# Performance work log

Hardware: AMD Instinct MI355X
Metric: run time of the kernel (lower is better)

## Reference

```python
import jax, jax.numpy as jnp
import numpy as np

B, H, W, C = 16, 56, 56, 512
HEADS, WIN = 16, 7
HID = 2048
EPS = 1e-5


def _rel_pos_index(win):
    coords = np.stack(np.meshgrid(np.arange(win), np.arange(win), indexing='ij'))  # 2,w,w
    cf = coords.reshape(2, -1)  # 2, w*w
    rel = (cf[:, :, None] - cf[:, None, :]).transpose(1, 2, 0).astype(np.int64)  # N,N,2
    rel[..., 0] += win - 1
    rel[..., 1] += win - 1
    rel[..., 0] *= 2 * win - 1
    return jnp.asarray(rel.sum(-1))  # N,N


def setup_inputs() -> dict:
    key = jax.random.key(0)
    ks = jax.random.split(key, 12)
    s = 0.02
    return {
        'x': jax.random.normal(ks[0], (B, H * W, C), jnp.float32),
        'norm1_w': jnp.ones((C,), jnp.float32),
        'norm1_b': jnp.zeros((C,), jnp.float32),
        'qkv_w': jax.random.normal(ks[1], (3 * C, C), jnp.float32) * s,
        'qkv_b': jnp.zeros((3 * C,), jnp.float32),
        'proj_w': jax.random.normal(ks[2], (C, C), jnp.float32) * s,
        'proj_b': jnp.zeros((C,), jnp.float32),
        'rel_bias_table': jax.random.normal(ks[3], ((2 * WIN - 1) ** 2, HEADS), jnp.float32) * s,
        'norm2_w': jnp.ones((C,), jnp.float32),
        'norm2_b': jnp.zeros((C,), jnp.float32),
        'fc1_w': jax.random.normal(ks[4], (HID, C), jnp.float32) * s,
        'fc1_b': jnp.zeros((HID,), jnp.float32),
        'fc2_w': jax.random.normal(ks[5], (C, HID), jnp.float32) * s,
        'fc2_b': jnp.zeros((C,), jnp.float32),
        'rel_pos_index': _rel_pos_index(WIN),
    }


def _ln(x, w, b):
    m = jnp.mean(x, -1, keepdims=True)
    v = jnp.mean((x - m) ** 2, -1, keepdims=True)
    return (x - m) * jax.lax.rsqrt(v + EPS) * w + b


def reference(x, norm1_w, norm1_b, qkv_w, qkv_b, proj_w, proj_b, rel_bias_table,
              norm2_w, norm2_b, fc1_w, fc1_b, fc2_w, fc2_b, rel_pos_index):
    N = WIN * WIN
    hd = C // HEADS
    shortcut = x
    h = _ln(x, norm1_w, norm1_b).reshape(B, H, W, C)
    # window partition -> (nW*B, N, C)
    h = h.reshape(B, H // WIN, WIN, W // WIN, WIN, C).transpose(0, 1, 3, 2, 4, 5)
    xw = h.reshape(-1, N, C)
    Bw = xw.shape[0]
    qkv = (xw @ qkv_w.T + qkv_b).reshape(Bw, N, 3, HEADS, hd).transpose(2, 0, 3, 1, 4)
    q, k, v = qkv[0], qkv[1], qkv[2]  # (Bw, heads, N, hd)
    q = q * (hd ** -0.5)
    attn = jnp.einsum('bhnd,bhmd->bhnm', q, k)
    bias = rel_bias_table[rel_pos_index.reshape(-1)].reshape(N, N, HEADS).transpose(2, 0, 1)
    attn = jax.nn.softmax(attn + bias[None], axis=-1)
    out = jnp.einsum('bhnm,bhmd->bhnd', attn, v).transpose(0, 2, 1, 3).reshape(Bw, N, C)
    out = out @ proj_w.T + proj_b
    # window reverse -> (B, H*W, C)
    out = out.reshape(B, H // WIN, W // WIN, WIN, WIN, C).transpose(0, 1, 3, 2, 4, 5)
    out = out.reshape(B, H * W, C)
    x = shortcut + out
    h2 = _ln(x, norm2_w, norm2_b)
    h2 = jax.nn.gelu(h2 @ fc1_w.T + fc1_b, approximate=False) @ fc2_w.T + fc2_b
    return x + h2
```

## Files before the change

### kernel.cpp

```cpp
#include <hip/hip_runtime.h>
#include <stdint.h>

#define B_    16
#define C_    512
#define HEADS 16
#define NTOK  49
#define ROWS  (16*56*56)

typedef __attribute__((ext_vector_type(8))) __bf16 bf16x8;
typedef __attribute__((ext_vector_type(4))) float  f32x4;
typedef __attribute__((ext_vector_type(8))) unsigned short u16x8;
typedef __attribute__((ext_vector_type(4))) unsigned short u16x4;

#define AS1 __attribute__((address_space(1)))
#define AS3 __attribute__((address_space(3)))

__device__ __forceinline__ unsigned short f2bf(float f) {
  union { float f; uint32_t u; } x; x.f = f;
  uint32_t r = x.u + 0x7FFFu + ((x.u >> 16) & 1u);
  return (unsigned short)(r >> 16);
}
__device__ __forceinline__ float bf2f(unsigned short u) {
  union { uint32_t u; float f; } x; x.u = ((uint32_t)u) << 16;
  return x.f;
}

__device__ __forceinline__ int winmap(int grow) {
  const int b = grow / 3136;
  const int pos = grow - b * 3136;
  const int y = pos / 56, x = pos - y * 56;
  const int win = (y / 7) * 8 + (x / 7);
  const int r = (y % 7) * 7 + (x % 7);
  return b * 3136 + win * 49 + r;
}

template<int EPI, int GATHER>
__global__ __launch_bounds__(256, 4)
void gemm_bt(const unsigned short* __restrict__ A,
             const unsigned short* __restrict__ Bt,
             const float* __restrict__ bias,
             const float* __restrict__ res,
             void* __restrict__ outp,
             int N, int K, int ldb, int nbn)
{
  __shared__ __align__(16) unsigned short As[2][128*32];
  __shared__ __align__(16) unsigned short Bs[2][128*32];

  const int nwg = gridDim.x;
  const int q8 = nwg >> 3, r8 = nwg & 7;
  const int xcd = blockIdx.x & 7, ixc = blockIdx.x >> 3;
  const int l = (xcd < r8 ? xcd * (q8 + 1) : r8 * (q8 + 1) + (xcd - r8) * q8) + ixc;
  const int bm = l / nbn, bn = l % nbn;

  const int tid  = threadIdx.x;
  const int wave = tid >> 6;
  const int lane = tid & 63;
  const int wr = wave >> 1, wc = wave & 1;

  const unsigned short* aSrc[2];
  const unsigned short* bSrc[2];
  #pragma unroll
  for (int i = 0; i < 2; ++i) {
    const int u = tid + i * 256;
    const int srow = u >> 2;
    const int sg   = (u & 3) ^ ((srow >> 1) & 3);
    int ga = bm * 128 + srow;
    if (GATHER) ga = winmap(ga);
    aSrc[i] = A  + (size_t)ga * K + sg * 8;
    bSrc[i] = Bt + (size_t)(bn * 128 + srow) * ldb + sg * 8;
  }

  f32x4 acc[4][4] = {};
  const int fr = lane & 15;
  const int kq = lane >> 4;
  const int xrd = kq ^ ((fr >> 1) & 3);

  auto STAGE = [&](int buf, int t) {
    const int k0 = t << 5;
    #pragma unroll
    for (int i = 0; i < 2; ++i)
      __builtin_amdgcn_global_load_lds(
        (const AS1 void*)(aSrc[i] + k0),
        (AS3 void*)(&As[buf][(i * 256 + wave * 64) * 8]), 16, 0, 0);
    #pragma unroll
    for (int i = 0; i < 2; ++i)
      __builtin_amdgcn_global_load_lds(
        (const AS1 void*)(bSrc[i] + k0),
        (AS3 void*)(&Bs[buf][(i * 256 + wave * 64) * 8]), 16, 0, 0);
  };

  const int nt = K >> 5;
  STAGE(0, 0);
  for (int t = 0; t < nt; ++t) {
    const int c = t & 1;
    if (t + 1 < nt) {
      STAGE(c ^ 1, t + 1);
      asm volatile("s_waitcnt vmcnt(4)" ::: "memory");
    } else {
      asm volatile("s_waitcnt vmcnt(0)" ::: "memory");
    }
    __builtin_amdgcn_s_barrier();
    asm volatile("" ::: "memory");

    bf16x8 a[4], b[4];
    #pragma unroll
    for (int m = 0; m < 4; ++m)
      a[m] = *(const bf16x8*)&As[c][(wr * 64 + m * 16 + fr) * 32 + xrd * 8];
    #pragma unroll
    for (int n = 0; n < 4; ++n)
      b[n] = *(const bf16x8*)&Bs[c][(wc * 64 + n * 16 + fr) * 32 + xrd * 8];

    __builtin_amdgcn_s_setprio(1);
    #pragma unroll
    for (int m = 0; m < 4; ++m)
      #pragma unroll
      for (int n = 0; n < 4; ++n)
        acc[m][n] = __builtin_amdgcn_mfma_f32_16x16x32_bf16(a[m], b[n], acc[m][n], 0, 0, 0);
    __builtin_amdgcn_s_setprio(0);

    asm volatile("s_waitcnt lgkmcnt(0)" ::: "memory");
    __builtin_amdgcn_s_barrier();
    asm volatile("" ::: "memory");
  }

  const int rq = lane >> 4;
  #pragma unroll
  for (int m = 0; m < 4; ++m) {
    #pragma unroll
    for (int n = 0; n < 4; ++n) {
      const int gcol = bn * 128 + wc * 64 + n * 16 + fr;
      const float bv = (EPI == 3) ? 0.f : bias[gcol];
      #pragma unroll
      for (int r = 0; r < 4; ++r) {
        const int grow = bm * 128 + wr * 64 + m * 16 + rq * 4 + r;
        const size_t off = (size_t)grow * N + gcol;
        float v = acc[m][n][r] + bv;
        if (EPI == 0) {
          ((unsigned short*)outp)[off] = f2bf(v);
        } else if (EPI == 1) {
          const float u2 = 1.5957691216f * v * (1.0f + 0.044715f * v * v);
          v = v / (1.0f + __expf(-u2));
          ((unsigned short*)outp)[off] = f2bf(v);
        } else {
          ((float*)outp)[off] = v + res[off];
        }
      }
    }
  }
}

__global__ __launch_bounds__(256)
void ln_bf16(const float* __restrict__ x, const float* __restrict__ w,
             const float* __restrict__ b, unsigned short* __restrict__ out)
{
  const int row  = blockIdx.x * 4 + (threadIdx.x >> 6);
  const int lane = threadIdx.x & 63;
  const float4* xr = (const float4*)(x + (size_t)row * C_);
  const float4 u = xr[lane * 2];
  const float4 v = xr[lane * 2 + 1];
  const float vals[8] = {u.x,u.y,u.z,u.w,v.x,v.y,v.z,v.w};
  float s = 0.f, s2 = 0.f;
  #pragma unroll
  for (int j = 0; j < 8; ++j) { s += vals[j]; s2 += vals[j]*vals[j]; }
  #pragma unroll
  for (int off = 1; off < 64; off <<= 1) {
    s  += __shfl_xor(s,  off);
    s2 += __shfl_xor(s2, off);
  }
  const float mean = s * (1.0f/512.0f);
  const float rstd = rsqrtf(s2 * (1.0f/512.0f) - mean*mean + 1e-5f);
  u16x8 o;
  #pragma unroll
  for (int j = 0; j < 8; ++j) {
    const int col = lane * 8 + j;
    o[j] = f2bf((vals[j] - mean) * rstd * w[col] + b[col]);
  }
  *(u16x8*)&out[(size_t)row * C_ + lane * 8] = o;
}

__global__ __launch_bounds__(256)
void attn_win3(const unsigned short* __restrict__ qkv,
               const unsigned short* __restrict__ biasBf,
               unsigned short* __restrict__ woutb, int i0)
{
  __shared__ float Ksh[4][NTOK*32];
  __shared__ float Vsh[4][NTOK*32];
  __shared__ unsigned short Bsh[4][NTOK*NTOK];
  const int bi = blockIdx.x;
  const int qtr = bi & 3, winl = bi >> 2;
  const int bbl = winl >> 6, wy = (winl >> 3) & 7, wx = winl & 7;
  const int wave = threadIdx.x >> 6, lane = threadIdx.x & 63;
  const int head = qtr * 4 + wave;

  for (int i = lane; i < NTOK*NTOK; i += 64)
    Bsh[wave][i] = biasBf[head * (NTOK*NTOK) + i];

  float q[32];
  if (lane < NTOK) {
    const int r = lane / 7, c = lane % 7;
    const size_t gl = (size_t)bbl * 3136 + (size_t)((wy*7 + r) * 56 + (wx*7 + c));
    const unsigned short* qp = qkv + gl * 1536 + head * 32;
    #pragma unroll
    for (int d = 0; d < 32; d += 4) {
      const u16x4 qv = *(const u16x4*)&qp[d];
      const u16x4 kv = *(const u16x4*)&qp[512 + d];
      const u16x4 vv = *(const u16x4*)&qp[1024 + d];
      #pragma unroll
      for (int e = 0; e < 4; ++e) {
        q[d+e] = bf2f(qv[e]);
        Ksh[wave][lane*32 + d + e] = bf2f(kv[e]);
        Vsh[wave][lane*32 + d + e] = bf2f(vv[e]);
      }
    }
  }
  if (lane < NTOK) {
    float lsum = 0.f;
    float o[32];
    #pragma unroll
    for (int d = 0; d < 32; ++d) o[d] = 0.f;
    for (int j = 0; j < NTOK; ++j) {
      float dot = 0.f;
      #pragma unroll
      for (int d = 0; d < 32; ++d) dot += q[d] * Ksh[wave][j*32 + d];
      const float val = dot * 0.17677669529663687f
                      + bf2f(Bsh[wave][lane*NTOK + j]);
      const float e = __expf(val);
      lsum += e;
      #pragma unroll
      for (int d = 0; d < 32; ++d) o[d] += e * Vsh[wave][j*32 + d];
    }
    const float inv = 1.0f / lsum;
    unsigned short* op = woutb
        + ((size_t)((bbl + i0) * 64 + wy * 8 + wx) * 49 + lane) * 512 + head * 32;
    #pragma unroll
    for (int d = 0; d < 32; d += 4) {
      u16x4 ov;
      #pragma unroll
      for (int e = 0; e < 4; ++e) ov[e] = f2bf(o[d+e] * inv);
      *(u16x4*)&op[d] = ov;
    }
  }
}

__global__ void build_bias(const float* __restrict__ table, const int* __restrict__ idx,
                           unsigned short* __restrict__ biasBf)
{
  const int i = blockIdx.x * 256 + threadIdx.x;
  if (i >= HEADS * NTOK * NTOK) return;
  const int h  = i / (NTOK*NTOK);
  const int ij = i - h * (NTOK*NTOK);
  biasBf[i] = f2bf(table[idx[ij] * HEADS + h]);
}

__global__ void conv_bf16(const float* __restrict__ in, unsigned short* __restrict__ out, int n4)
{
  const int i = blockIdx.x * 256 + threadIdx.x;
  if (i >= n4) return;
  const float4 v = ((const float4*)in)[i];
  u16x4 o; o[0]=f2bf(v.x); o[1]=f2bf(v.y); o[2]=f2bf(v.z); o[3]=f2bf(v.w);
  ((u16x4*)out)[i] = o;
}

extern "C" void kernel_launch(void* const* d_in, const int* in_sizes, int n_in,
                              void* d_out, int out_size, void* d_ws, size_t ws_size,
                              hipStream_t stream)
{
  const float* x     = (const float*)d_in[0];
  const float* n1w   = (const float*)d_in[1];
  const float* n1b   = (const float*)d_in[2];
  const float* qkvw  = (const float*)d_in[3];
  const float* qkvb  = (const float*)d_in[4];
  const float* projw = (const float*)d_in[5];
  const float* projb = (const float*)d_in[6];
  const float* rbt   = (const float*)d_in[7];
  const float* n2w   = (const float*)d_in[8];
  const float* n2b   = (const float*)d_in[9];
  const float* fc1w  = (const float*)d_in[10];
  const float* fc1b  = (const float*)d_in[11];
  const float* fc2w  = (const float*)d_in[12];
  const float* fc2b  = (const float*)d_in[13];
  const int*   rpi   = (const int*)d_in[14];
  float* out = (float*)d_out;

  char* p = (char*)d_ws;
  auto alloc = [&](size_t bytes) -> char* {
    char* q = p; p += (bytes + 255) & ~(size_t)255; return q;
  };
  unsigned short* wqB  = (unsigned short*)alloc((size_t)1536 * 512 * 2);
  unsigned short* wpB  = (unsigned short*)alloc((size_t)512  * 512 * 2);
  unsigned short* w1B  = (unsigned short*)alloc((size_t)2048 * 512 * 2);
  unsigned short* w2B  = (unsigned short*)alloc((size_t)512  * 2048 * 2);
  unsigned short* biasBf = (unsigned short*)alloc((size_t)HEADS * NTOK * NTOK * 2);
  unsigned short* bufX = (unsigned short*)alloc((size_t)ROWS * 512 * 2);
  const size_t used = (size_t)(p - (char*)d_ws);
  const size_t Rbytes = (ws_size > used) ? ws_size - used : 0;
  unsigned short* R = (unsigned short*)p;

  int ic = 0;
  for (int c = 16; c >= 2; c >>= 1)
    if ((size_t)c * 3136 * 1536 * 2 <= Rbytes) { ic = c; break; }
  int hc = 0;
  for (int c = 2048; c >= 128; c >>= 1)
    if ((size_t)ROWS * c * 2 <= Rbytes) { hc = c; break; }
  if (ic == 0 || hc == 0) return;

  conv_bf16<<<(1536*512/4 + 255)/256, 256, 0, stream>>>(qkvw, wqB, 1536*512/4);
  conv_bf16<<<(512*512/4  + 255)/256, 256, 0, stream>>>(projw, wpB, 512*512/4);
  conv_bf16<<<(2048*512/4 + 255)/256, 256, 0, stream>>>(fc1w, w1B, 2048*512/4);
  conv_bf16<<<(512*2048/4 + 255)/256, 256, 0, stream>>>(fc2w, w2B, 512*2048/4);
  build_bias<<<(HEADS*NTOK*NTOK + 255)/256, 256, 0, stream>>>(rbt, rpi, biasBf);

  ln_bf16<<<ROWS/4, 256, 0, stream>>>(x, n1w, n1b, bufX);

  for (int i0 = 0; i0 < B_; i0 += ic) {
    const int nbm = ic * 3136 / 128, nbn = 12;
    gemm_bt<0,0><<<nbm * nbn, 256, 0, stream>>>(
        bufX + (size_t)i0*3136*512, wqB, qkvb, nullptr, R, 1536, 512, 512, nbn);
    attn_win3<<<ic*64*4, 256, 0, stream>>>(R, biasBf, bufX, i0);
  }

  gemm_bt<2,1><<<(ROWS/128) * 4, 256, 0, stream>>>(
      bufX, wpB, projb, x, out, 512, 512, 512, 4);

  ln_bf16<<<ROWS/4, 256, 0, stream>>>(out, n2w, n2b, bufX);

  for (int h0 = 0; h0 < 2048; h0 += hc) {
    gemm_bt<1,0><<<(ROWS/128) * (hc/128), 256, 0, stream>>>(
        bufX, w1B + (size_t)h0*512, fc1b + h0, nullptr, R, hc, 512, 512, hc/128);
    if (h0 == 0)
      gemm_bt<2,0><<<(ROWS/128) * 4, 256, 0, stream>>>(
          R, w2B + h0, fc2b, out, out, 512, hc, 2048, 4);
    else
      gemm_bt<3,0><<<(ROWS/128) * 4, 256, 0, stream>>>(
          R, w2B + h0, nullptr, out, out, 512, hc, 2048, 4);
  }
}
```

Baseline: 717.9 us.

## Enlarge GEMM tiles to 256x256 with 8 waves and phased K=64 pipeline

The bf16 GEMM moves from 128x128 tiles with 4 waves and K-step 32 to 256x256 tiles with 8 waves (512 threads) and K-step 64. Each step is split into four phases that interleave LDS fragment reads, async global-to-LDS prefetch of the next stage, and MFMA blocks, with barriers between phases. The aim is more data reuse per loaded byte and better overlap of memory traffic with matrix math. In exchange it uses more LDS and registers (the acc array doubles), launches fewer workgroups, and adds more barriers. Host launch grids and chunk-size minimums are updated to match.

Result: slower. 759.1 us (+5.7%).

```diff
diff --git a/kernel.cpp b/kernel.cpp
--- a/kernel.cpp
+++ b/kernel.cpp
@@ -35,7 +35,7 @@
 }
 
 template<int EPI, int GATHER>
-__global__ __launch_bounds__(256, 4)
+__global__ __launch_bounds__(512, 2)
 void gemm_bt(const unsigned short* __restrict__ A,
              const unsigned short* __restrict__ Bt,
              const float* __restrict__ bias,
@@ -43,8 +43,8 @@
              void* __restrict__ outp,
              int N, int K, int ldb, int nbn)
 {
-  __shared__ __align__(16) unsigned short As[2][128*32];
-  __shared__ __align__(16) unsigned short Bs[2][128*32];
+  __shared__ __align__(16) unsigned short As[2][2 * 8192];
+  __shared__ __align__(16) unsigned short Bs[2][2 * 8192];
 
   const int nwg = gridDim.x;
   const int q8 = nwg >> 3, r8 = nwg & 7;
@@ -55,84 +55,102 @@
   const int tid  = threadIdx.x;
   const int wave = tid >> 6;
   const int lane = tid & 63;
-  const int wr = wave >> 1, wc = wave & 1;
-
-  const unsigned short* aSrc[2];
-  const unsigned short* bSrc[2];
+  const int wr = wave >> 2, wc = wave & 3;
+
+  const unsigned short* aP[2];
+  const unsigned short* bP[2];
   #pragma unroll
   for (int i = 0; i < 2; ++i) {
-    const int u = tid + i * 256;
-    const int srow = u >> 2;
-    const int sg   = (u & 3) ^ ((srow >> 1) & 3);
-    int ga = bm * 128 + srow;
+    const int u = i * 512 + tid;
+    const int row = u >> 2;
+    const int g = (u & 3) ^ ((row >> 1) & 3);
+    int ga = bm * 256 + row;
     if (GATHER) ga = winmap(ga);
-    aSrc[i] = A  + (size_t)ga * K + sg * 8;
-    bSrc[i] = Bt + (size_t)(bn * 128 + srow) * ldb + sg * 8;
-  }
-
-  f32x4 acc[4][4] = {};
+    aP[i] = A  + (size_t)ga * K + g * 8;
+    bP[i] = Bt + (size_t)(bn * 256 + row) * ldb + g * 8;
+  }
+
+  f32x4 acc[8][4] = {};
   const int fr = lane & 15;
   const int kq = lane >> 4;
   const int xrd = kq ^ ((fr >> 1) & 3);
 
-  auto STAGE = [&](int buf, int t) {
-    const int k0 = t << 5;
-    #pragma unroll
-    for (int i = 0; i < 2; ++i)
-      __builtin_amdgcn_global_load_lds(
-        (const AS1 void*)(aSrc[i] + k0),
-        (AS3 void*)(&As[buf][(i * 256 + wave * 64) * 8]), 16, 0, 0);
-    #pragma unroll
-    for (int i = 0; i < 2; ++i)
-      __builtin_amdgcn_global_load_lds(
-        (const AS1 void*)(bSrc[i] + k0),
-        (AS3 void*)(&Bs[buf][(i * 256 + wave * 64) * 8]), 16, 0, 0);
+  auto STAGE = [&](int buf, int t, int which) {
+    const int kh = which >> 1;
+    const int k0 = (t << 6) + kh * 32;
+    if (which & 1) {
+      #pragma unroll
+      for (int i = 0; i < 2; ++i)
+        __builtin_amdgcn_global_load_lds(
+          (const AS1 void*)(bP[i] + k0),
+          (AS3 void*)(&Bs[buf][kh * 8192 + (i * 512 + wave * 64) * 8]), 16, 0, 0);
+    } else {
+      #pragma unroll
+      for (int i = 0; i < 2; ++i)
+        __builtin_amdgcn_global_load_lds(
+          (const AS1 void*)(aP[i] + k0),
+          (AS3 void*)(&As[buf][kh * 8192 + (i * 512 + wave * 64) * 8]), 16, 0, 0);
+    }
   };
 
-  const int nt = K >> 5;
-  STAGE(0, 0);
+  const int nt = K >> 6;
+  STAGE(0, 0, 0); STAGE(0, 0, 1); STAGE(0, 0, 2); STAGE(0, 0, 3);
+  asm volatile("s_waitcnt vmcnt(4)" ::: "memory");
+  __builtin_amdgcn_s_barrier();
+
   for (int t = 0; t < nt; ++t) {
-    const int c = t & 1;
-    if (t + 1 < nt) {
-      STAGE(c ^ 1, t + 1);
-      asm volatile("s_waitcnt vmcnt(4)" ::: "memory");
-    } else {
-      asm volatile("s_waitcnt vmcnt(0)" ::: "memory");
-    }
-    __builtin_amdgcn_s_barrier();
-    asm volatile("" ::: "memory");
-
-    bf16x8 a[4], b[4];
-    #pragma unroll
-    for (int m = 0; m < 4; ++m)
-      a[m] = *(const bf16x8*)&As[c][(wr * 64 + m * 16 + fr) * 32 + xrd * 8];
-    #pragma unroll
-    for (int n = 0; n < 4; ++n)
-      b[n] = *(const bf16x8*)&Bs[c][(wc * 64 + n * 16 + fr) * 32 + xrd * 8];
-
-    __builtin_amdgcn_s_setprio(1);
-    #pragma unroll
-    for (int m = 0; m < 4; ++m)
-      #pragma unroll
-      for (int n = 0; n < 4; ++n)
-        acc[m][n] = __builtin_amdgcn_mfma_f32_16x16x32_bf16(a[m], b[n], acc[m][n], 0, 0, 0);
-    __builtin_amdgcn_s_setprio(0);
-
-    asm volatile("s_waitcnt lgkmcnt(0)" ::: "memory");
-    __builtin_amdgcn_s_barrier();
-    asm volatile("" ::: "memory");
+    const int cur = t & 1, nxt = cur ^ 1;
+    const bool more = (t + 1 < nt);
+    bf16x8 b[4];
+
+    #pragma unroll
+    for (int ph = 0; ph < 4; ++ph) {
+      const int ks = ph >> 1, mh = ph & 1;
+
+      bf16x8 a[4];
+      #pragma unroll
+      for (int m = 0; m < 4; ++m)
+        a[m] = *(const bf16x8*)&As[cur][ks * 8192
+                  + (wr * 128 + (mh * 4 + m) * 16 + fr) * 32 + xrd * 8];
+      if (mh == 0) {
+        #pragma unroll
+        for (int n = 0; n < 4; ++n)
+          b[n] = *(const bf16x8*)&Bs[cur][ks * 8192
+                    + (wc * 64 + n * 16 + fr) * 32 + xrd * 8];
+      }
+      if (more) STAGE(nxt, t + 1, ph);
+
+      __builtin_amdgcn_s_barrier();
+      asm volatile("s_waitcnt lgkmcnt(0)" ::: "memory");
+      __builtin_amdgcn_s_setprio(1);
+      #pragma unroll
+      for (int m = 0; m < 4; ++m)
+        #pragma unroll
+        for (int n = 0; n < 4; ++n)
+          acc[mh * 4 + m][n] =
+            __builtin_amdgcn_mfma_f32_16x16x32_bf16(a[m], b[n], acc[mh * 4 + m][n], 0, 0, 0);
+      __builtin_amdgcn_s_setprio(0);
+
+      if (ph == 1) {
+        if (more) asm volatile("s_waitcnt vmcnt(4)" ::: "memory");
+        else      asm volatile("s_waitcnt vmcnt(0)" ::: "memory");
+      } else if (ph == 3) {
+        if (more) asm volatile("s_waitcnt vmcnt(4)" ::: "memory");
+      }
+      __builtin_amdgcn_s_barrier();
+    }
   }
 
   const int rq = lane >> 4;
   #pragma unroll
-  for (int m = 0; m < 4; ++m) {
+  for (int m = 0; m < 8; ++m) {
     #pragma unroll
     for (int n = 0; n < 4; ++n) {
-      const int gcol = bn * 128 + wc * 64 + n * 16 + fr;
+      const int gcol = bn * 256 + wc * 64 + n * 16 + fr;
       const float bv = (EPI == 3) ? 0.f : bias[gcol];
       #pragma unroll
       for (int r = 0; r < 4; ++r) {
-        const int grow = bm * 128 + wr * 64 + m * 16 + rq * 4 + r;
+        const int grow = bm * 256 + wr * 128 + m * 16 + rq * 4 + r;
         const size_t off = (size_t)grow * N + gcol;
         float v = acc[m][n][r] + bv;
         if (EPI == 0) {
@@ -297,10 +315,10 @@
   unsigned short* R = (unsigned short*)p;
 
   int ic = 0;
-  for (int c = 16; c >= 2; c >>= 1)
+  for (int c = 16; c >= 4; c >>= 1)
     if ((size_t)c * 3136 * 1536 * 2 <= Rbytes) { ic = c; break; }
   int hc = 0;
-  for (int c = 2048; c >= 128; c >>= 1)
+  for (int c = 2048; c >= 256; c >>= 1)
     if ((size_t)ROWS * c * 2 <= Rbytes) { hc = c; break; }
   if (ic == 0 || hc == 0) return;
 
@@ -313,25 +331,25 @@
   ln_bf16<<<ROWS/4, 256, 0, stream>>>(x, n1w, n1b, bufX);
 
   for (int i0 = 0; i0 < B_; i0 += ic) {
-    const int nbm = ic * 3136 / 128, nbn = 12;
-    gemm_bt<0,0><<<nbm * nbn, 256, 0, stream>>>(
+    const int nbm = ic * 3136 / 256, nbn = 6;
+    gemm_bt<0,0><<<nbm * nbn, 512, 0, stream>>>(
         bufX + (size_t)i0*3136*512, wqB, qkvb, nullptr, R, 1536, 512, 512, nbn);
     attn_win3<<<ic*64*4, 256, 0, stream>>>(R, biasBf, bufX, i0);
   }
 
-  gemm_bt<2,1><<<(ROWS/128) * 4, 256, 0, stream>>>(
-      bufX, wpB, projb, x, out, 512, 512, 512, 4);
+  gemm_bt<2,1><<<(ROWS/256) * 2, 512, 0, stream>>>(
+      bufX, wpB, projb, x, out, 512, 512, 512, 2);
 
   ln_bf16<<<ROWS/4, 256, 0, stream>>>(out, n2w, n2b, bufX);
 
   for (int h0 = 0; h0 < 2048; h0 += hc) {
-    gemm_bt<1,0><<<(ROWS/128) * (hc/128), 256, 0, stream>>>(
-        bufX, w1B + (size_t)h0*512, fc1b + h0, nullptr, R, hc, 512, 512, hc/128);
+    gemm_bt<1,0><<<(ROWS/256) * (hc/256), 512, 0, stream>>>(
+        bufX, w1B + (size_t)h0*512, fc1b + h0, nullptr, R, hc, 512, 512, hc/256);
     if (h0 == 0)
-      gemm_bt<2,0><<<(ROWS/128) * 4, 256, 0, stream>>>(
-          R, w2B + h0, fc2b, out, out, 512, hc, 2048, 4);
+      gemm_bt<2,0><<<(ROWS/256) * 2, 512, 0, stream>>>(
+          R, w2B + h0, fc2b, out, out, 512, hc, 2048, 2);
     else
-      gemm_bt<3,0><<<(ROWS/128) * 4, 256, 0, stream>>>(
-          R, w2B + h0, nullptr, out, out, 512, hc, 2048, 4);
-  }
-}
+      gemm_bt<3,0><<<(ROWS/256) * 2, 512, 0, stream>>>(
+          R, w2B + h0, nullptr, out, out, 512, hc, 2048, 2);
+  }
+}
```

## Load GEMM A operand directly from global into registers, bypassing LDS

Applied to the files above, without the earlier changes.

The GEMM no longer stages the A tile through shared memory. Each wave loads its own A fragments straight from global memory into registers, prefetching one k-step ahead. B keeps its double-buffered LDS staging, and the k-loop is unrolled by two to ping-pong the A register sets. This halves LDS use and removes the LDS reads for A, at the cost of duplicated A fetches across waves that share rows, narrower 64-byte row segments per load, and higher register pressure; launch bounds are relaxed from 4 to 3 waves per SIMD to allow for this.

After: 986.5 us. 37.4% more time.

```diff
diff --git a/kernel.cpp b/kernel.cpp
--- a/kernel.cpp
+++ b/kernel.cpp
@@ -35,7 +35,7 @@
 }
 
 template<int EPI, int GATHER>
-__global__ __launch_bounds__(256, 4)
+__global__ __launch_bounds__(256, 3)
 void gemm_bt(const unsigned short* __restrict__ A,
              const unsigned short* __restrict__ Bt,
              const float* __restrict__ bias,
@@ -43,7 +43,6 @@
              void* __restrict__ outp,
              int N, int K, int ldb, int nbn)
 {
-  __shared__ __align__(16) unsigned short As[2][128*32];
   __shared__ __align__(16) unsigned short Bs[2][128*32];
 
   const int nwg = gridDim.x;
@@ -57,31 +56,31 @@
   const int lane = tid & 63;
   const int wr = wave >> 1, wc = wave & 1;
 
-  const unsigned short* aSrc[2];
+  const int fr = lane & 15;
+  const int kq = lane >> 4;
+  const int xrd = kq ^ ((fr >> 1) & 3);
+
   const unsigned short* bSrc[2];
   #pragma unroll
   for (int i = 0; i < 2; ++i) {
     const int u = tid + i * 256;
     const int srow = u >> 2;
     const int sg   = (u & 3) ^ ((srow >> 1) & 3);
-    int ga = bm * 128 + srow;
-    if (GATHER) ga = winmap(ga);
-    aSrc[i] = A  + (size_t)ga * K + sg * 8;
     bSrc[i] = Bt + (size_t)(bn * 128 + srow) * ldb + sg * 8;
   }
 
+  const unsigned short* aRow[4];
+  #pragma unroll
+  for (int m = 0; m < 4; ++m) {
+    int r = bm * 128 + wr * 64 + m * 16 + fr;
+    if (GATHER) r = winmap(r);
+    aRow[m] = A + (size_t)r * K + kq * 8;
+  }
+
   f32x4 acc[4][4] = {};
-  const int fr = lane & 15;
-  const int kq = lane >> 4;
-  const int xrd = kq ^ ((fr >> 1) & 3);
-
-  auto STAGE = [&](int buf, int t) {
+
+  auto STAGE_B = [&](int buf, int t) {
     const int k0 = t << 5;
-    #pragma unroll
-    for (int i = 0; i < 2; ++i)
-      __builtin_amdgcn_global_load_lds(
-        (const AS1 void*)(aSrc[i] + k0),
-        (AS3 void*)(&As[buf][(i * 256 + wave * 64) * 8]), 16, 0, 0);
     #pragma unroll
     for (int i = 0; i < 2; ++i)
       __builtin_amdgcn_global_load_lds(
@@ -89,39 +88,48 @@
         (AS3 void*)(&Bs[buf][(i * 256 + wave * 64) * 8]), 16, 0, 0);
   };
 
+  bf16x8 aA[4], aB[4];
+  STAGE_B(0, 0);
+  #pragma unroll
+  for (int m = 0; m < 4; ++m) aA[m] = *(const bf16x8*)(aRow[m]);
+
   const int nt = K >> 5;
-  STAGE(0, 0);
-  for (int t = 0; t < nt; ++t) {
-    const int c = t & 1;
-    if (t + 1 < nt) {
-      STAGE(c ^ 1, t + 1);
-      asm volatile("s_waitcnt vmcnt(4)" ::: "memory");
-    } else {
-      asm volatile("s_waitcnt vmcnt(0)" ::: "memory");
-    }
-    __builtin_amdgcn_s_barrier();
-    asm volatile("" ::: "memory");
-
-    bf16x8 a[4], b[4];
-    #pragma unroll
-    for (int m = 0; m < 4; ++m)
-      a[m] = *(const bf16x8*)&As[c][(wr * 64 + m * 16 + fr) * 32 + xrd * 8];
-    #pragma unroll
-    for (int n = 0; n < 4; ++n)
-      b[n] = *(const bf16x8*)&Bs[c][(wc * 64 + n * 16 + fr) * 32 + xrd * 8];
-
-    __builtin_amdgcn_s_setprio(1);
-    #pragma unroll
-    for (int m = 0; m < 4; ++m)
-      #pragma unroll
-      for (int n = 0; n < 4; ++n)
-        acc[m][n] = __builtin_amdgcn_mfma_f32_16x16x32_bf16(a[m], b[n], acc[m][n], 0, 0, 0);
-    __builtin_amdgcn_s_setprio(0);
-
-    asm volatile("s_waitcnt lgkmcnt(0)" ::: "memory");
-    __builtin_amdgcn_s_barrier();
-    asm volatile("" ::: "memory");
-  }
+
+#define GEMM_ITER(c, t, aCur, aNxt, MORE)                                     \
+  {                                                                           \
+    if (MORE) {                                                               \
+      STAGE_B((c) ^ 1, (t) + 1);                                              \
+      const int k1 = ((t) + 1) << 5;                                          \
+      _Pragma("unroll")                                                       \
+      for (int m = 0; m < 4; ++m) aNxt[m] = *(const bf16x8*)(aRow[m] + k1);   \
+      asm volatile("s_waitcnt vmcnt(6)" ::: "memory");                        \
+    } else {                                                                  \
+      asm volatile("s_waitcnt vmcnt(0)" ::: "memory");                        \
+    }                                                                         \
+    __builtin_amdgcn_s_barrier();                                             \
+    asm volatile("" ::: "memory");                                            \
+    bf16x8 b[4];                                                              \
+    _Pragma("unroll")                                                         \
+    for (int n = 0; n < 4; ++n)                                               \
+      b[n] = *(const bf16x8*)&Bs[c][(wc * 64 + n * 16 + fr) * 32 + xrd * 8];  \
+    __builtin_amdgcn_s_setprio(1);                                            \
+    _Pragma("unroll")                                                         \
+    for (int m = 0; m < 4; ++m)                                               \
+      _Pragma("unroll")                                                       \
+      for (int n = 0; n < 4; ++n)                                             \
+        acc[m][n] = __builtin_amdgcn_mfma_f32_16x16x32_bf16(aCur[m], b[n],    \
+                                                            acc[m][n], 0, 0, 0); \
+    __builtin_amdgcn_s_setprio(0);                                            \
+    asm volatile("s_waitcnt lgkmcnt(0)" ::: "memory");                        \
+    __builtin_amdgcn_s_barrier();                                             \
+    asm volatile("" ::: "memory");                                            \
+  }
+
+  for (int t = 0; t < nt; t += 2) {
+    GEMM_ITER(0, t,     aA, aB, true);
+    GEMM_ITER(1, t + 1, aB, aA, (t + 2 < nt));
+  }
+#undef GEMM_ITER
 
   const int rq = lane >> 4;
   #pragma unroll
```

## Fuse projection GEMM with residual add and LayerNorm2, write attention in place

Applied to the files above, without the earlier changes.

Adds a proj_ln kernel that computes a full 128x512 output row tile per block. It fuses the projection GEMM, bias, residual add and the second LayerNorm, writing both the fp32 residual output and the bf16 normalized activations. Attention now writes its output in place into the Q slice of the qkv buffer in image order, so the projection no longer needs a window-gather and the separate ln_bf16 pass and its extra read of the residual are removed. The new kernel uses 512 threads and a large accumulator set, which may reduce occupancy, and the projection now runs per batch chunk inside the attention loop.

Result: slower. 738.5 us (+2.9%).

```diff
diff --git a/kernel.cpp b/kernel.cpp
--- a/kernel.cpp
+++ b/kernel.cpp
@@ -25,16 +25,7 @@
   return x.f;
 }
 
-__device__ __forceinline__ int winmap(int grow) {
-  const int b = grow / 3136;
-  const int pos = grow - b * 3136;
-  const int y = pos / 56, x = pos - y * 56;
-  const int win = (y / 7) * 8 + (x / 7);
-  const int r = (y % 7) * 7 + (x % 7);
-  return b * 3136 + win * 49 + r;
-}
-
-template<int EPI, int GATHER>
+template<int EPI>
 __global__ __launch_bounds__(256, 4)
 void gemm_bt(const unsigned short* __restrict__ A,
              const unsigned short* __restrict__ Bt,
@@ -64,9 +55,7 @@
     const int u = tid + i * 256;
     const int srow = u >> 2;
     const int sg   = (u & 3) ^ ((srow >> 1) & 3);
-    int ga = bm * 128 + srow;
-    if (GATHER) ga = winmap(ga);
-    aSrc[i] = A  + (size_t)ga * K + sg * 8;
+    aSrc[i] = A  + (size_t)(bm * 128 + srow) * K + sg * 8;
     bSrc[i] = Bt + (size_t)(bn * 128 + srow) * ldb + sg * 8;
   }
 
@@ -149,6 +138,152 @@
   }
 }
 
+__global__ __launch_bounds__(512, 2)
+void proj_ln(const unsigned short* __restrict__ Aq,
+             const unsigned short* __restrict__ Bt,
+             const float* __restrict__ bias,
+             const float* __restrict__ xres,
+             const float* __restrict__ nw, const float* __restrict__ nb,
+             float* __restrict__ outF,
+             unsigned short* __restrict__ outLn)
+{
+  __shared__ __align__(16) unsigned short As[2][128*32];
+  __shared__ __align__(16) unsigned short Bs[2][512*32];
+  __shared__ float red[128][4][2];
+
+  const int bm = blockIdx.x;
+  const int tid  = threadIdx.x;
+  const int wave = tid >> 6;
+  const int lane = tid & 63;
+  const int wr = wave >> 2, wc = wave & 3;
+
+  const int fr = lane & 15;
+  const int kq = lane >> 4;
+  const int xrd = kq ^ ((fr >> 1) & 3);
+
+  const int au = tid, arow = au >> 2;
+  const int ag = (au & 3) ^ ((arow >> 1) & 3);
+  const unsigned short* aSrc = Aq + (size_t)(bm * 128 + arow) * 1536 + ag * 8;
+  const unsigned short* bSrc[4];
+  #pragma unroll
+  for (int i = 0; i < 4; ++i) {
+    const int u = i * 512 + tid;
+    const int row = u >> 2;
+    const int g = (u & 3) ^ ((row >> 1) & 3);
+    bSrc[i] = Bt + (size_t)row * 512 + g * 8;
+  }
+
+  f32x4 acc[4][8] = {};
+
+  auto STAGE = [&](int buf, int t) {
+    const int k0 = t << 5;
+    __builtin_amdgcn_global_load_lds(
+      (const AS1 void*)(aSrc + k0),
+      (AS3 void*)(&As[buf][(wave * 64) * 8]), 16, 0, 0);
+    #pragma unroll
+    for (int i = 0; i < 4; ++i)
+      __builtin_amdgcn_global_load_lds(
+        (const AS1 void*)(bSrc[i] + k0),
+        (AS3 void*)(&Bs[buf][(i * 512 + wave * 64) * 8]), 16, 0, 0);
+  };
+
+  const int nt = 16;
+  STAGE(0, 0);
+  for (int t = 0; t < nt; ++t) {
+    const int c = t & 1;
+    if (t + 1 < nt) {
+      STAGE(c ^ 1, t + 1);
+      asm volatile("s_waitcnt vmcnt(5)" ::: "memory");
+    } else {
+      asm volatile("s_waitcnt vmcnt(0)" ::: "memory");
+    }
+    __builtin_amdgcn_s_barrier();
+    asm volatile("" ::: "memory");
+
+    bf16x8 a[4], b[8];
+    #pragma unroll
+    for (int m = 0; m < 4; ++m)
+      a[m] = *(const bf16x8*)&As[c][(wr * 64 + m * 16 + fr) * 32 + xrd * 8];
+    #pragma unroll
+    for (int n = 0; n < 8; ++n)
+      b[n] = *(const bf16x8*)&Bs[c][(wc * 128 + n * 16 + fr) * 32 + xrd * 8];
+
+    __builtin_amdgcn_s_setprio(1);
+    #pragma unroll
+    for (int m = 0; m < 4; ++m)
+      #pragma unroll
+      for (int n = 0; n < 8; ++n)
+        acc[m][n] = __builtin_amdgcn_mfma_f32_16x16x32_bf16(a[m], b[n], acc[m][n], 0, 0, 0);
+    __builtin_amdgcn_s_setprio(0);
+
+    asm volatile("s_waitcnt lgkmcnt(0)" ::: "memory");
+    __builtin_amdgcn_s_barrier();
+    asm volatile("" ::: "memory");
+  }
+
+  const int rq = lane >> 4;
+  float nwv[8], nbv[8], bv[8];
+  #pragma unroll
+  for (int n = 0; n < 8; ++n) {
+    const int gcol = wc * 128 + n * 16 + fr;
+    nwv[n] = nw[gcol]; nbv[n] = nb[gcol]; bv[n] = bias[gcol];
+  }
+
+  float s1[4][4], s2[4][4];
+  #pragma unroll
+  for (int m = 0; m < 4; ++m) {
+    #pragma unroll
+    for (int r = 0; r < 4; ++r) {
+      const int growl = bm * 128 + wr * 64 + m * 16 + rq * 4 + r;
+      float s = 0.f, ss = 0.f;
+      #pragma unroll
+      for (int n = 0; n < 8; ++n) {
+        const int gcol = wc * 128 + n * 16 + fr;
+        float v = acc[m][n][r] + bv[n] + xres[(size_t)growl * 512 + gcol];
+        acc[m][n][r] = v;
+        s += v; ss += v * v;
+      }
+      #pragma unroll
+      for (int off = 1; off < 16; off <<= 1) {
+        s  += __shfl_xor(s,  off);
+        ss += __shfl_xor(ss, off);
+      }
+      s1[m][r] = s; s2[m][r] = ss;
+    }
+  }
+  if (fr == 0) {
+    #pragma unroll
+    for (int m = 0; m < 4; ++m)
+      #pragma unroll
+      for (int r = 0; r < 4; ++r) {
+        const int rl = wr * 64 + m * 16 + rq * 4 + r;
+        red[rl][wc][0] = s1[m][r];
+        red[rl][wc][1] = s2[m][r];
+      }
+  }
+  __syncthreads();
+
+  #pragma unroll
+  for (int m = 0; m < 4; ++m) {
+    #pragma unroll
+    for (int r = 0; r < 4; ++r) {
+      const int rl = wr * 64 + m * 16 + rq * 4 + r;
+      const float S  = red[rl][0][0] + red[rl][1][0] + red[rl][2][0] + red[rl][3][0];
+      const float SS = red[rl][0][1] + red[rl][1][1] + red[rl][2][1] + red[rl][3][1];
+      const float mean = S * (1.0f / 512.0f);
+      const float rstd = rsqrtf(SS * (1.0f / 512.0f) - mean * mean + 1e-5f);
+      const size_t rowoff = (size_t)(bm * 128 + rl) * 512;
+      #pragma unroll
+      for (int n = 0; n < 8; ++n) {
+        const int gcol = wc * 128 + n * 16 + fr;
+        const float v = acc[m][n][r];
+        outF[rowoff + gcol] = v;
+        outLn[rowoff + gcol] = f2bf((v - mean) * rstd * nwv[n] + nbv[n]);
+      }
+    }
+  }
+}
+
 __global__ __launch_bounds__(256)
 void ln_bf16(const float* __restrict__ x, const float* __restrict__ w,
              const float* __restrict__ b, unsigned short* __restrict__ out)
@@ -179,9 +314,8 @@
 }
 
 __global__ __launch_bounds__(256)
-void attn_win3(const unsigned short* __restrict__ qkv,
-               const unsigned short* __restrict__ biasBf,
-               unsigned short* __restrict__ woutb, int i0)
+void attn_win3(unsigned short* __restrict__ qkv,
+               const unsigned short* __restrict__ biasBf)
 {
   __shared__ float Ksh[4][NTOK*32];
   __shared__ float Vsh[4][NTOK*32];
@@ -196,9 +330,10 @@
     Bsh[wave][i] = biasBf[head * (NTOK*NTOK) + i];
 
   float q[32];
+  size_t gl = 0;
   if (lane < NTOK) {
     const int r = lane / 7, c = lane % 7;
-    const size_t gl = (size_t)bbl * 3136 + (size_t)((wy*7 + r) * 56 + (wx*7 + c));
+    gl = (size_t)bbl * 3136 + (size_t)((wy*7 + r) * 56 + (wx*7 + c));
     const unsigned short* qp = qkv + gl * 1536 + head * 32;
     #pragma unroll
     for (int d = 0; d < 32; d += 4) {
@@ -230,8 +365,7 @@
       for (int d = 0; d < 32; ++d) o[d] += e * Vsh[wave][j*32 + d];
     }
     const float inv = 1.0f / lsum;
-    unsigned short* op = woutb
-        + ((size_t)((bbl + i0) * 64 + wy * 8 + wx) * 49 + lane) * 512 + head * 32;
+    unsigned short* op = qkv + gl * 1536 + head * 32;
     #pragma unroll
     for (int d = 0; d < 32; d += 4) {
       u16x4 ov;
@@ -313,25 +447,24 @@
   ln_bf16<<<ROWS/4, 256, 0, stream>>>(x, n1w, n1b, bufX);
 
   for (int i0 = 0; i0 < B_; i0 += ic) {
+    const size_t roff = (size_t)i0 * 3136;
     const int nbm = ic * 3136 / 128, nbn = 12;
-    gemm_bt<0,0><<<nbm * nbn, 256, 0, stream>>>(
-        bufX + (size_t)i0*3136*512, wqB, qkvb, nullptr, R, 1536, 512, 512, nbn);
-    attn_win3<<<ic*64*4, 256, 0, stream>>>(R, biasBf, bufX, i0);
-  }
-
-  gemm_bt<2,1><<<(ROWS/128) * 4, 256, 0, stream>>>(
-      bufX, wpB, projb, x, out, 512, 512, 512, 4);
-
-  ln_bf16<<<ROWS/4, 256, 0, stream>>>(out, n2w, n2b, bufX);
+    gemm_bt<0><<<nbm * nbn, 256, 0, stream>>>(
+        bufX + roff * 512, wqB, qkvb, nullptr, R, 1536, 512, 512, nbn);
+    attn_win3<<<ic*64*4, 256, 0, stream>>>(R, biasBf);
+    proj_ln<<<nbm, 512, 0, stream>>>(
+        R, wpB, projb, x + roff * 512, n2w, n2b,
+        out + roff * 512, bufX + roff * 512);
+  }
 
   for (int h0 = 0; h0 < 2048; h0 += hc) {
-    gemm_bt<1,0><<<(ROWS/128) * (hc/128), 256, 0, stream>>>(
+    gemm_bt<1><<<(ROWS/128) * (hc/128), 256, 0, stream>>>(
         bufX, w1B + (size_t)h0*512, fc1b + h0, nullptr, R, hc, 512, 512, hc/128);
     if (h0 == 0)
-      gemm_bt<2,0><<<(ROWS/128) * 4, 256, 0, stream>>>(
+      gemm_bt<2><<<(ROWS/128) * 4, 256, 0, stream>>>(
           R, w2B + h0, fc2b, out, out, 512, hc, 2048, 4);
     else
-      gemm_bt<3,0><<<(ROWS/128) * 4, 256, 0, stream>>>(
+      gemm_bt<3><<<(ROWS/128) * 4, 256, 0, stream>>>(
           R, w2B + h0, nullptr, out, out, 512, hc, 2048, 4);
   }
 }
```
